# Kernel optimization log

Hardware: AMD Instinct MI355X
Metric: run time of the kernel (lower is better)

The kernel has to match this reference:

```python
import jax, jax.numpy as jnp
import numpy as np

B, T, D, H = 1024, 128, 128, 8
HS = D // H  # 16, matches the hard-coded 16**-0.5 scale
EPS = 1e-5


def setup_inputs() -> dict:
    key = jax.random.key(0)
    ks = jax.random.split(key, 12)
    s = 0.02
    return {
        "x": jax.random.normal(ks[0], (B, T, D), jnp.float32),
        "Wq": jax.random.normal(ks[1], (H, D, HS), jnp.float32) * s,
        "Wk": jax.random.normal(ks[2], (H, D, HS), jnp.float32) * s,
        "Wv": jax.random.normal(ks[3], (H, D, HS), jnp.float32) * s,
        "Wo": jax.random.normal(ks[4], (D, D), jnp.float32) * s,
        "bo": jnp.zeros((D,), jnp.float32),
        "W1": jax.random.normal(ks[5], (D, 4 * D), jnp.float32) * s,
        "b1": jnp.zeros((4 * D,), jnp.float32),
        "W2": jax.random.normal(ks[6], (4 * D, D), jnp.float32) * s,
        "b2": jnp.zeros((D,), jnp.float32),
        "g1": jnp.ones((D,), jnp.float32),
        "be1": jnp.zeros((D,), jnp.float32),
        "g2": jnp.ones((D,), jnp.float32),
        "be2": jnp.zeros((D,), jnp.float32),
    }


def _layernorm(x, g, b):
    mu = jnp.mean(x, axis=-1, keepdims=True)
    var = jnp.mean(jnp.square(x - mu), axis=-1, keepdims=True)
    return (x - mu) * jax.lax.rsqrt(var + EPS) * g + b


def _block(x, Wq, Wk, Wv, Wo, bo, W1, b1, W2, b2, g1, be1, g2, be2):
    h = _layernorm(x, g1, be1)
    q = jnp.einsum('btd,hde->bhte', h, Wq)
    k = jnp.einsum('btd,hde->bhte', h, Wk)
    v = jnp.einsum('btd,hde->bhte', h, Wv)
    scores = jnp.einsum('bhte,bhse->bhts', q, k) * (16.0 ** -0.5)
    causal = jnp.tril(jnp.ones((T, T), bool))
    scores = jnp.where(causal, scores, -jnp.inf)
    wei = jax.nn.softmax(scores, axis=-1)  # dropout off (eval)
    o = jnp.einsum('bhts,bhse->bhte', wei, v)
    o = jnp.transpose(o, (0, 2, 1, 3)).reshape(x.shape[0], T, D)  # concat heads
    x = x + (o @ Wo + bo)
    h2 = _layernorm(x, g2, be2)
    ff = jax.nn.relu(h2 @ W1 + b1) @ W2 + b2
    return x + ff


def reference(x, Wq, Wk, Wv, Wo, bo, W1, b1, W2, b2, g1, be1, g2, be2):
    return _block(x, Wq, Wk, Wv, Wo, bo, W1, b1, W2, b2, g1, be1, g2, be2)
```

## Files before the change

### kernel.cpp

```cpp
#include <hip/hip_runtime.h>
#include <hip/hip_bf16.h>

typedef unsigned short u16;
typedef unsigned int u32;
typedef __bf16 bf16x8 __attribute__((ext_vector_type(8)));
typedef float f32x4 __attribute__((ext_vector_type(4)));

#define LDA 136

__device__ __forceinline__ u16 f2b(float f) {
  __bf16 b = (__bf16)f;
  return __builtin_bit_cast(u16, b);
}
__device__ __forceinline__ float b2f(u16 h) {
  u32 u = ((u32)h) << 16;
  return __builtin_bit_cast(float, u);
}
__device__ __forceinline__ u32 pk2(float lo, float hi) {
  return (u32)f2b(lo) | ((u32)f2b(hi) << 16);
}
__device__ __forceinline__ bf16x8 zero8() {
  union { int4 i; bf16x8 v; } u;
  u.i = make_int4(0, 0, 0, 0);
  return u.v;
}
__device__ __forceinline__ f32x4 mfma16(bf16x8 a, bf16x8 b, f32x4 c) {
  return __builtin_amdgcn_mfma_f32_16x16x32_bf16(a, b, c, 0, 0, 0);
}

__device__ __forceinline__ bf16x8 gatherB(const f32x4& ve, const f32x4& vo,
                                          bool odd_valid, float scale,
                                          int l15, int lg) {
  u32 pe0 = pk2(ve[0] * scale, ve[1] * scale);
  u32 pe1 = pk2(ve[2] * scale, ve[3] * scale);
  u32 po0 = 0, po1 = 0;
  if (odd_valid) {
    po0 = pk2(vo[0] * scale, vo[1] * scale);
    po1 = pk2(vo[2] * scale, vo[3] * scale);
  }
  int s0 = ((lg & 1) * 2) * 16 + l15;
  u32 a0 = __shfl(pe0, s0),      a1 = __shfl(pe1, s0);
  u32 a2 = __shfl(pe0, s0 + 16), a3 = __shfl(pe1, s0 + 16);
  u32 b0 = __shfl(po0, s0),      b1 = __shfl(po1, s0);
  u32 b2 = __shfl(po0, s0 + 16), b3 = __shfl(po1, s0 + 16);
  union { u32 u[4]; bf16x8 v; } fr;
  bool lo = (lg < 2);
  fr.u[0] = lo ? a0 : b0; fr.u[1] = lo ? a1 : b1;
  fr.u[2] = lo ? a2 : b2; fr.u[3] = lo ? a3 : b3;
  return fr.v;
}

__global__ void prep_kernel(const float* __restrict__ Wq, const float* __restrict__ Wk,
                            const float* __restrict__ Wv, const float* __restrict__ Wo,
                            const float* __restrict__ W1, const float* __restrict__ W2,
                            u16* __restrict__ o) {
  int i = blockIdx.x * 256 + threadIdx.x;
  if (i >= 196608) return;
  float v;
  if (i < 49152) {
    int which = i >> 14, j = i & 16383;
    int n = j >> 7, k = j & 127;
    const float* W = (which == 0) ? Wq : (which == 1) ? Wk : Wv;
    v = W[((n >> 4) * 128 + k) * 16 + (n & 15)];
  } else if (i < 65536) {
    int j = i - 49152;
    v = Wo[(j & 127) * 128 + (j >> 7)];
  } else if (i < 131072) {
    int j = i - 65536;
    v = W1[(j & 127) * 512 + (j >> 7)];
  } else {
    int j = i - 131072;
    int c = j & 127, r = (j >> 7) & 15, nt = (j >> 11) & 7, cc = j >> 14;
    v = W2[(cc * 128 + c) * 128 + nt * 16 + r];
  }
  o[i] = f2b(v);
}

__device__ __forceinline__ void ln_regs(const float (&v)[8][4], const float* __restrict__ g,
                                        const float* __restrict__ be,
                                        u16* __restrict__ dst, int r0, int l15) {
  #pragma unroll
  for (int rg = 0; rg < 4; ++rg) {
    float s = 0.f;
    #pragma unroll
    for (int nt = 0; nt < 8; ++nt) s += v[nt][rg];
    s += __shfl_xor(s, 1); s += __shfl_xor(s, 2);
    s += __shfl_xor(s, 4); s += __shfl_xor(s, 8);
    float mu = s * 0.0078125f;
    float vv = 0.f;
    #pragma unroll
    for (int nt = 0; nt < 8; ++nt) { float d = v[nt][rg] - mu; vv += d * d; }
    vv += __shfl_xor(vv, 1); vv += __shfl_xor(vv, 2);
    vv += __shfl_xor(vv, 4); vv += __shfl_xor(vv, 8);
    float rs = rsqrtf(vv * 0.0078125f + 1e-5f);
    #pragma unroll
    for (int nt = 0; nt < 8; ++nt) {
      int col = nt * 16 + l15;
      dst[(r0 + rg) * LDA + col] = f2b((v[nt][rg] - mu) * rs * g[col] + be[col]);
    }
  }
}

__global__ void __launch_bounds__(512, 4)
tblock_kernel(const float* __restrict__ xg, const u16* __restrict__ wts,
              const float* __restrict__ bo, const float* __restrict__ b1,
              const float* __restrict__ b2, const float* __restrict__ g1,
              const float* __restrict__ be1, const float* __restrict__ g2,
              const float* __restrict__ be2, float* __restrict__ out) {
  extern __shared__ u16 sm[];
  u16* buf1 = sm;
  u16* buf2 = sm + 128 * LDA;

  const int tid  = threadIdx.x;
  const int w    = tid >> 6;
  const int lane = tid & 63;
  const int l15  = lane & 15;
  const int lg   = lane >> 4;
  const int r0   = w * 16 + lg * 4;

  const u16* WqT = wts;
  const u16* WkT = wts + 16384;
  const u16* WvT = wts + 32768;
  const u16* WoT = wts + 49152;
  const u16* W1T = wts + 65536;
  const u16* W2S = wts + 131072;

  const float* xp = xg + (size_t)blockIdx.x * 16384;
  float*       op = out + (size_t)blockIdx.x * 16384;

  const f32x4 zf4 = {0.f, 0.f, 0.f, 0.f};
  const bf16x8 zb8 = zero8();

  {
    float xr[8][4];
    #pragma unroll
    for (int nt = 0; nt < 8; ++nt)
      #pragma unroll
      for (int rg = 0; rg < 4; ++rg)
        xr[nt][rg] = xp[(r0 + rg) * 128 + nt * 16 + l15];
    ln_regs(xr, g1, be1, buf1, r0, l15);
  }
  __syncthreads();

  bf16x8 av[4];
  {
    bf16x8 bw[4];
    #pragma unroll
    for (int kk = 0; kk < 4; ++kk)
      bw[kk] = *(const bf16x8*)(WvT + (w * 16 + l15) * 128 + kk * 32 + lg * 8);
    f32x4 va[8];
    #pragma unroll
    for (int mt = 0; mt < 8; ++mt) {
      va[mt] = zf4;
      #pragma unroll
      for (int kk = 0; kk < 4; ++kk)
        va[mt] = mfma16(*(const bf16x8*)(buf1 + (mt * 16 + l15) * LDA + kk * 32 + lg * 8),
                        bw[kk], va[mt]);
    }
    #pragma unroll
    for (int kk = 0; kk < 4; ++kk)
      av[kk] = gatherB(va[2 * kk], va[2 * kk + 1], true, 1.f, l15, lg);
  }

  bf16x8 bk[8];
  {
    bf16x8 bw[4];
    #pragma unroll
    for (int kk = 0; kk < 4; ++kk)
      bw[kk] = *(const bf16x8*)(WkT + (w * 16 + l15) * 128 + kk * 32 + lg * 8);
    f32x4 ka[8];
    #pragma unroll
    for (int mt = 0; mt < 8; ++mt) {
      ka[mt] = zf4;
      #pragma unroll
      for (int kk = 0; kk < 4; ++kk)
        ka[mt] = mfma16(*(const bf16x8*)(buf1 + (mt * 16 + l15) * LDA + kk * 32 + lg * 8),
                        bw[kk], ka[mt]);
    }
    #pragma unroll
    for (int mt = 0; mt < 8; ++mt)
      #pragma unroll
      for (int rg = 0; rg < 4; ++rg)
        buf2[(mt * 16 + lg * 4 + rg) * LDA + w * 16 + l15] = f2b(ka[mt][rg]);
  }
  __syncthreads();
  #pragma unroll
  for (int st = 0; st < 8; ++st) {
    bk[st] = zb8;
    if (lg < 2) bk[st] = *(const bf16x8*)(buf2 + (st * 16 + l15) * LDA + w * 16 + lg * 8);
  }
  __syncthreads();

  {
    bf16x8 bw[4];
    #pragma unroll
    for (int kk = 0; kk < 4; ++kk)
      bw[kk] = *(const bf16x8*)(WqT + (w * 16 + l15) * 128 + kk * 32 + lg * 8);
    f32x4 qa[8];
    #pragma unroll
    for (int mt = 0; mt < 8; ++mt) {
      qa[mt] = zf4;
      #pragma unroll
      for (int kk = 0; kk < 4; ++kk)
        qa[mt] = mfma16(*(const bf16x8*)(buf1 + (mt * 16 + l15) * LDA + kk * 32 + lg * 8),
                        bw[kk], qa[mt]);
    }
    #pragma unroll
    for (int mt = 0; mt < 8; ++mt)
      #pragma unroll
      for (int rg = 0; rg < 4; ++rg)
        buf2[(mt * 16 + lg * 4 + rg) * LDA + w * 16 + l15] = f2b(qa[mt][rg]);
  }
  __syncthreads();

  #pragma unroll 1
  for (int mt = 0; mt < 8; ++mt) {
    bf16x8 aq = zb8;
    if (lg < 2) aq = *(const bf16x8*)(buf2 + (mt * 16 + l15) * LDA + w * 16 + lg * 8);

    f32x4 sacc[8];
    #pragma unroll
    for (int st = 0; st < 8; ++st)
      sacc[st] = (st <= mt) ? mfma16(bk[st], aq, zf4) : zf4;

    float mx = -3.0e38f;
    #pragma unroll
    for (int st = 0; st < 8; ++st) if (st <= mt) {
      #pragma unroll
      for (int rg = 0; rg < 4; ++rg) {
        float sv = sacc[st][rg] * 0.25f;
        bool ok = (st < mt) || ((lg * 4 + rg) <= l15);
        sv = ok ? sv : -1.0e30f;
        sacc[st][rg] = sv;
        mx = fmaxf(mx, sv);
      }
    }
    mx = fmaxf(mx, __shfl_xor(mx, 16));
    mx = fmaxf(mx, __shfl_xor(mx, 32));
    float sum = 0.f;
    #pragma unroll
    for (int st = 0; st < 8; ++st) if (st <= mt) {
      #pragma unroll
      for (int rg = 0; rg < 4; ++rg) {
        float e = __expf(sacc[st][rg] - mx);
        sacc[st][rg] = e;
        sum += e;
      }
    }
    sum += __shfl_xor(sum, 16);
    sum += __shfl_xor(sum, 32);
    float inv = 1.f / sum;

    f32x4 oacc = zf4;
    #pragma unroll
    for (int kk = 0; kk < 4; ++kk) if (kk <= (mt >> 1)) {
      bf16x8 fr = gatherB(sacc[2 * kk], sacc[2 * kk + 1], (2 * kk + 1) <= mt, inv, l15, lg);
      oacc = mfma16(av[kk], fr, oacc);
    }
    union { u16 h[4]; ushort4 s4; } ow;
    #pragma unroll
    for (int rg = 0; rg < 4; ++rg) ow.h[rg] = f2b(oacc[rg]);
    *(ushort4*)(buf2 + (mt * 16 + l15) * LDA + w * 16 + lg * 4) = ow.s4;
  }
  __syncthreads();

  {
    bf16x8 bw[4];
    #pragma unroll
    for (int kk = 0; kk < 4; ++kk)
      bw[kk] = *(const bf16x8*)(WoT + (w * 16 + l15) * 128 + kk * 32 + lg * 8);
    float bov = bo[w * 16 + l15];
    #pragma unroll
    for (int mt = 0; mt < 8; ++mt) {
      float xrl[4];
      #pragma unroll
      for (int rg = 0; rg < 4; ++rg)
        xrl[rg] = xp[(mt * 16 + lg * 4 + rg) * 128 + w * 16 + l15];
      f32x4 acc = zf4;
      #pragma unroll
      for (int kk = 0; kk < 4; ++kk)
        acc = mfma16(*(const bf16x8*)(buf2 + (mt * 16 + l15) * LDA + kk * 32 + lg * 8),
                     bw[kk], acc);
      #pragma unroll
      for (int rg = 0; rg < 4; ++rg) {
        float x1v = acc[rg] + bov + xrl[rg];
        int row = mt * 16 + lg * 4 + rg;
        op[row * 128 + w * 16 + l15] = x1v;
        buf1[row * LDA + w * 16 + l15] = f2b(x1v);
      }
    }
  }
  __syncthreads();

  {
    int rw  = w * 16 + (lane >> 2);
    int sub = lane & 3;
    u16* rp = buf1 + rw * LDA;
    float tv[32];
    float s = 0.f;
    #pragma unroll
    for (int j = 0; j < 32; ++j) { tv[j] = b2f(rp[sub + 4 * j]); s += tv[j]; }
    s += __shfl_xor(s, 1); s += __shfl_xor(s, 2);
    float mu = s * 0.0078125f;
    float vv = 0.f;
    #pragma unroll
    for (int j = 0; j < 32; ++j) { float d = tv[j] - mu; vv += d * d; }
    vv += __shfl_xor(vv, 1); vv += __shfl_xor(vv, 2);
    float rs = rsqrtf(vv * 0.0078125f + 1e-5f);
    #pragma unroll
    for (int j = 0; j < 32; ++j) {
      int c = sub + 4 * j;
      rp[c] = f2b((tv[j] - mu) * rs * g2[c] + be2[c]);
    }
  }
  __syncthreads();

  {
    f32x4 oacc2[8];
    #pragma unroll
    for (int mt = 0; mt < 8; ++mt) oacc2[mt] = zf4;

    #pragma unroll 1
    for (int cc = 0; cc < 4; ++cc) {
      bf16x8 bw1[4];
      #pragma unroll
      for (int kk = 0; kk < 4; ++kk)
        bw1[kk] = *(const bf16x8*)(W1T + (cc * 128 + w * 16 + l15) * 128 + kk * 32 + lg * 8);
      float b1v = b1[cc * 128 + w * 16 + l15];
      #pragma unroll
      for (int mt = 0; mt < 8; ++mt) {
        f32x4 facc = zf4;
        #pragma unroll
        for (int kk = 0; kk < 4; ++kk)
          facc = mfma16(*(const bf16x8*)(buf1 + (mt * 16 + l15) * LDA + kk * 32 + lg * 8),
                        bw1[kk], facc);
        #pragma unroll
        for (int rg = 0; rg < 4; ++rg)
          buf2[(mt * 16 + lg * 4 + rg) * LDA + w * 16 + l15] =
              f2b(fmaxf(facc[rg] + b1v, 0.f));
      }
      __syncthreads();

      bf16x8 bw2[4];
      #pragma unroll
      for (int kk = 0; kk < 4; ++kk)
        bw2[kk] = *(const bf16x8*)(W2S + ((cc * 8 + w) * 16 + l15) * 128 + kk * 32 + lg * 8);
      #pragma unroll
      for (int mt = 0; mt < 8; ++mt)
        #pragma unroll
        for (int kk = 0; kk < 4; ++kk)
          oacc2[mt] = mfma16(*(const bf16x8*)(buf2 + (mt * 16 + l15) * LDA + kk * 32 + lg * 8),
                             bw2[kk], oacc2[mt]);
      __syncthreads();
    }

    float b2v = b2[w * 16 + l15];
    #pragma unroll
    for (int mt = 0; mt < 8; ++mt) {
      float x1r[4];
      #pragma unroll
      for (int rg = 0; rg < 4; ++rg)
        x1r[rg] = op[(mt * 16 + lg * 4 + rg) * 128 + w * 16 + l15];
      #pragma unroll
      for (int rg = 0; rg < 4; ++rg)
        op[(mt * 16 + lg * 4 + rg) * 128 + w * 16 + l15] = oacc2[mt][rg] + b2v + x1r[rg];
    }
  }
}

extern "C" void kernel_launch(void* const* d_in, const int* in_sizes, int n_in,
                              void* d_out, int out_size, void* d_ws, size_t ws_size,
                              hipStream_t stream) {
  const float* x   = (const float*)d_in[0];
  const float* Wq  = (const float*)d_in[1];
  const float* Wk  = (const float*)d_in[2];
  const float* Wv  = (const float*)d_in[3];
  const float* Wo  = (const float*)d_in[4];
  const float* bo  = (const float*)d_in[5];
  const float* W1  = (const float*)d_in[6];
  const float* b1  = (const float*)d_in[7];
  const float* W2  = (const float*)d_in[8];
  const float* b2  = (const float*)d_in[9];
  const float* g1  = (const float*)d_in[10];
  const float* be1 = (const float*)d_in[11];
  const float* g2  = (const float*)d_in[12];
  const float* be2 = (const float*)d_in[13];
  u16* wts = (u16*)d_ws;

  prep_kernel<<<768, 256, 0, stream>>>(Wq, Wk, Wv, Wo, W1, W2, wts);

  const int smem_bytes = 2 * 128 * LDA * 2;
  hipFuncSetAttribute(reinterpret_cast<const void*>(tblock_kernel),
                      hipFuncAttributeMaxDynamicSharedMemorySize, smem_bytes);
  tblock_kernel<<<1024, 512, smem_bytes, stream>>>(x, wts, bo, b1, b2, g1, be1, g2,
                                                   be2, (float*)d_out);
}
```

Baseline: 144.6 us.

## Retile GEMMs as 2x4 warp grid with transposed MFMA and vectorized IO

Each warp now owns a 64-row by 32-column output tile for the Wo, W1 and W2 GEMMs instead of a 16-column strip over all 128 rows. Operand order is swapped so accumulators map to contiguous columns, which allows float4 and ushort4 global and LDS accesses. Q/K/V projections are fused into one pass over the LN output with fewer barriers. The first residual is kept in registers rather than written to and re-read from global, and W2 is re-laid out. Register pressure rises with the larger per-warp tiles, which could lower occupancy.

```diff
diff --git a/kernel.cpp b/kernel.cpp
--- a/kernel.cpp
+++ b/kernel.cpp
@@ -26,6 +26,10 @@
 }
 __device__ __forceinline__ f32x4 mfma16(bf16x8 a, bf16x8 b, f32x4 c) {
   return __builtin_amdgcn_mfma_f32_16x16x32_bf16(a, b, c, 0, 0, 0);
+}
+__device__ __forceinline__ ushort4 pk4(float a, float b, float c, float d) {
+  ushort4 r; r.x = f2b(a); r.y = f2b(b); r.z = f2b(c); r.w = f2b(d);
+  return r;
 }
 
 __device__ __forceinline__ bf16x8 gatherB(const f32x4& ve, const f32x4& vo,
@@ -70,35 +74,10 @@
     v = W1[(j & 127) * 512 + (j >> 7)];
   } else {
     int j = i - 131072;
-    int c = j & 127, r = (j >> 7) & 15, nt = (j >> 11) & 7, cc = j >> 14;
-    v = W2[(cc * 128 + c) * 128 + nt * 16 + r];
+    int c = j >> 9, n = j & 511;
+    v = W2[n * 128 + c];
   }
   o[i] = f2b(v);
-}
-
-__device__ __forceinline__ void ln_regs(const float (&v)[8][4], const float* __restrict__ g,
-                                        const float* __restrict__ be,
-                                        u16* __restrict__ dst, int r0, int l15) {
-  #pragma unroll
-  for (int rg = 0; rg < 4; ++rg) {
-    float s = 0.f;
-    #pragma unroll
-    for (int nt = 0; nt < 8; ++nt) s += v[nt][rg];
-    s += __shfl_xor(s, 1); s += __shfl_xor(s, 2);
-    s += __shfl_xor(s, 4); s += __shfl_xor(s, 8);
-    float mu = s * 0.0078125f;
-    float vv = 0.f;
-    #pragma unroll
-    for (int nt = 0; nt < 8; ++nt) { float d = v[nt][rg] - mu; vv += d * d; }
-    vv += __shfl_xor(vv, 1); vv += __shfl_xor(vv, 2);
-    vv += __shfl_xor(vv, 4); vv += __shfl_xor(vv, 8);
-    float rs = rsqrtf(vv * 0.0078125f + 1e-5f);
-    #pragma unroll
-    for (int nt = 0; nt < 8; ++nt) {
-      int col = nt * 16 + l15;
-      dst[(r0 + rg) * LDA + col] = f2b((v[nt][rg] - mu) * rs * g[col] + be[col]);
-    }
-  }
 }
 
 __global__ void __launch_bounds__(512, 4)
@@ -116,14 +95,17 @@
   const int lane = tid & 63;
   const int l15  = lane & 15;
   const int lg   = lane >> 4;
-  const int r0   = w * 16 + lg * 4;
-
-  const u16* WqT = wts;
-  const u16* WkT = wts + 16384;
-  const u16* WvT = wts + 32768;
-  const u16* WoT = wts + 49152;
-  const u16* W1T = wts + 65536;
-  const u16* W2S = wts + 131072;
+  const int mr   = w >> 2;
+  const int nc   = w & 3;
+  const int tr0  = mr * 64;
+  const int cb   = nc * 32;
+
+  const u16* WqT  = wts;
+  const u16* WkT  = wts + 16384;
+  const u16* WvT  = wts + 32768;
+  const u16* WoT  = wts + 49152;
+  const u16* W1T  = wts + 65536;
+  const u16* W2T2 = wts + 131072;
 
   const float* xp = xg + (size_t)blockIdx.x * 16384;
   float*       op = out + (size_t)blockIdx.x * 16384;
@@ -132,91 +114,89 @@
   const bf16x8 zb8 = zero8();
 
   {
-    float xr[8][4];
+    const int t = w * 16 + l15;
+    float v[8][4];
+    #pragma unroll
+    for (int nt = 0; nt < 8; ++nt) {
+      float4 f = *(const float4*)(xp + t * 128 + nt * 16 + lg * 4);
+      v[nt][0] = f.x; v[nt][1] = f.y; v[nt][2] = f.z; v[nt][3] = f.w;
+    }
+    float s = 0.f;
     #pragma unroll
     for (int nt = 0; nt < 8; ++nt)
       #pragma unroll
-      for (int rg = 0; rg < 4; ++rg)
-        xr[nt][rg] = xp[(r0 + rg) * 128 + nt * 16 + l15];
-    ln_regs(xr, g1, be1, buf1, r0, l15);
+      for (int r = 0; r < 4; ++r) s += v[nt][r];
+    s += __shfl_xor(s, 16); s += __shfl_xor(s, 32);
+    float mu = s * 0.0078125f;
+    float vv = 0.f;
+    #pragma unroll
+    for (int nt = 0; nt < 8; ++nt)
+      #pragma unroll
+      for (int r = 0; r < 4; ++r) { float d = v[nt][r] - mu; vv += d * d; }
+    vv += __shfl_xor(vv, 16); vv += __shfl_xor(vv, 32);
+    float rs = rsqrtf(vv * 0.0078125f + 1e-5f);
+    #pragma unroll
+    for (int nt = 0; nt < 8; ++nt) {
+      float4 gv = *(const float4*)(g1 + nt * 16 + lg * 4);
+      float4 bv = *(const float4*)(be1 + nt * 16 + lg * 4);
+      *(ushort4*)(buf1 + t * LDA + nt * 16 + lg * 4) =
+          pk4((v[nt][0] - mu) * rs * gv.x + bv.x, (v[nt][1] - mu) * rs * gv.y + bv.y,
+              (v[nt][2] - mu) * rs * gv.z + bv.z, (v[nt][3] - mu) * rs * gv.w + bv.w);
+    }
   }
   __syncthreads();
 
   bf16x8 av[4];
-  {
-    bf16x8 bw[4];
-    #pragma unroll
-    for (int kk = 0; kk < 4; ++kk)
-      bw[kk] = *(const bf16x8*)(WvT + (w * 16 + l15) * 128 + kk * 32 + lg * 8);
-    f32x4 va[8];
-    #pragma unroll
-    for (int mt = 0; mt < 8; ++mt) {
-      va[mt] = zf4;
-      #pragma unroll
-      for (int kk = 0; kk < 4; ++kk)
-        va[mt] = mfma16(*(const bf16x8*)(buf1 + (mt * 16 + l15) * LDA + kk * 32 + lg * 8),
-                        bw[kk], va[mt]);
-    }
-    #pragma unroll
-    for (int kk = 0; kk < 4; ++kk)
-      av[kk] = gatherB(va[2 * kk], va[2 * kk + 1], true, 1.f, l15, lg);
-  }
-
   bf16x8 bk[8];
   {
-    bf16x8 bw[4];
-    #pragma unroll
-    for (int kk = 0; kk < 4; ++kk)
-      bw[kk] = *(const bf16x8*)(WkT + (w * 16 + l15) * 128 + kk * 32 + lg * 8);
-    f32x4 ka[8];
+    bf16x8 wq[4], wk[4], wv[4];
+    #pragma unroll
+    for (int kk = 0; kk < 4; ++kk) {
+      wq[kk] = *(const bf16x8*)(WqT + (w * 16 + l15) * 128 + kk * 32 + lg * 8);
+      wk[kk] = *(const bf16x8*)(WkT + (w * 16 + l15) * 128 + kk * 32 + lg * 8);
+      wv[kk] = *(const bf16x8*)(WvT + (w * 16 + l15) * 128 + kk * 32 + lg * 8);
+    }
+    u32 qp[8][2];
+    f32x4 vprev = zf4;
     #pragma unroll
     for (int mt = 0; mt < 8; ++mt) {
-      ka[mt] = zf4;
+      bf16x8 hf[4];
       #pragma unroll
       for (int kk = 0; kk < 4; ++kk)
-        ka[mt] = mfma16(*(const bf16x8*)(buf1 + (mt * 16 + l15) * LDA + kk * 32 + lg * 8),
-                        bw[kk], ka[mt]);
-    }
-    #pragma unroll
-    for (int mt = 0; mt < 8; ++mt)
-      #pragma unroll
-      for (int rg = 0; rg < 4; ++rg)
-        buf2[(mt * 16 + lg * 4 + rg) * LDA + w * 16 + l15] = f2b(ka[mt][rg]);
-  }
-  __syncthreads();
-  #pragma unroll
-  for (int st = 0; st < 8; ++st) {
-    bk[st] = zb8;
-    if (lg < 2) bk[st] = *(const bf16x8*)(buf2 + (st * 16 + l15) * LDA + w * 16 + lg * 8);
-  }
-  __syncthreads();
-
-  {
-    bf16x8 bw[4];
-    #pragma unroll
-    for (int kk = 0; kk < 4; ++kk)
-      bw[kk] = *(const bf16x8*)(WqT + (w * 16 + l15) * 128 + kk * 32 + lg * 8);
-    f32x4 qa[8];
+        hf[kk] = *(const bf16x8*)(buf1 + (mt * 16 + l15) * LDA + kk * 32 + lg * 8);
+      f32x4 va = zf4, ka = zf4, qa = zf4;
+      #pragma unroll
+      for (int kk = 0; kk < 4; ++kk) {
+        va = mfma16(hf[kk], wv[kk], va);
+        ka = mfma16(wk[kk], hf[kk], ka);
+        qa = mfma16(wq[kk], hf[kk], qa);
+      }
+      *(ushort4*)(buf2 + (mt * 16 + l15) * LDA + w * 16 + lg * 4) =
+          pk4(ka[0], ka[1], ka[2], ka[3]);
+      qp[mt][0] = pk2(qa[0], qa[1]);
+      qp[mt][1] = pk2(qa[2], qa[3]);
+      if (mt & 1) av[mt >> 1] = gatherB(vprev, va, true, 1.f, l15, lg);
+      else        vprev = va;
+    }
+    #pragma unroll
+    for (int st = 0; st < 8; ++st) {
+      bk[st] = zb8;
+      if (lg < 2)
+        bk[st] = *(const bf16x8*)(buf2 + (st * 16 + l15) * LDA + w * 16 + lg * 8);
+    }
     #pragma unroll
     for (int mt = 0; mt < 8; ++mt) {
-      qa[mt] = zf4;
-      #pragma unroll
-      for (int kk = 0; kk < 4; ++kk)
-        qa[mt] = mfma16(*(const bf16x8*)(buf1 + (mt * 16 + l15) * LDA + kk * 32 + lg * 8),
-                        bw[kk], qa[mt]);
-    }
-    #pragma unroll
-    for (int mt = 0; mt < 8; ++mt)
-      #pragma unroll
-      for (int rg = 0; rg < 4; ++rg)
-        buf2[(mt * 16 + lg * 4 + rg) * LDA + w * 16 + l15] = f2b(qa[mt][rg]);
-  }
-  __syncthreads();
+      union { u32 u[2]; ushort4 s; } uq;
+      uq.u[0] = qp[mt][0]; uq.u[1] = qp[mt][1];
+      *(ushort4*)(buf2 + (mt * 16 + l15) * LDA + w * 16 + lg * 4) = uq.s;
+    }
+  }
 
   #pragma unroll 1
   for (int mt = 0; mt < 8; ++mt) {
     bf16x8 aq = zb8;
-    if (lg < 2) aq = *(const bf16x8*)(buf2 + (mt * 16 + l15) * LDA + w * 16 + lg * 8);
+    if (lg < 2)
+      aq = *(const bf16x8*)(buf2 + (mt * 16 + l15) * LDA + w * 16 + lg * 8);
 
     f32x4 sacc[8];
     #pragma unroll
@@ -257,113 +237,148 @@
       bf16x8 fr = gatherB(sacc[2 * kk], sacc[2 * kk + 1], (2 * kk + 1) <= mt, inv, l15, lg);
       oacc = mfma16(av[kk], fr, oacc);
     }
-    union { u16 h[4]; ushort4 s4; } ow;
-    #pragma unroll
-    for (int rg = 0; rg < 4; ++rg) ow.h[rg] = f2b(oacc[rg]);
-    *(ushort4*)(buf2 + (mt * 16 + l15) * LDA + w * 16 + lg * 4) = ow.s4;
+    *(ushort4*)(buf2 + (mt * 16 + l15) * LDA + w * 16 + lg * 4) =
+        pk4(oacc[0], oacc[1], oacc[2], oacc[3]);
   }
   __syncthreads();
 
+  f32x4 x1r[4][2];
   {
-    bf16x8 bw[4];
-    #pragma unroll
-    for (int kk = 0; kk < 4; ++kk)
-      bw[kk] = *(const bf16x8*)(WoT + (w * 16 + l15) * 128 + kk * 32 + lg * 8);
-    float bov = bo[w * 16 + l15];
-    #pragma unroll
-    for (int mt = 0; mt < 8; ++mt) {
-      float xrl[4];
-      #pragma unroll
-      for (int rg = 0; rg < 4; ++rg)
-        xrl[rg] = xp[(mt * 16 + lg * 4 + rg) * 128 + w * 16 + l15];
-      f32x4 acc = zf4;
+    bf16x8 wo[2][4];
+    #pragma unroll
+    for (int ct = 0; ct < 2; ++ct)
       #pragma unroll
       for (int kk = 0; kk < 4; ++kk)
-        acc = mfma16(*(const bf16x8*)(buf2 + (mt * 16 + l15) * LDA + kk * 32 + lg * 8),
-                     bw[kk], acc);
-      #pragma unroll
-      for (int rg = 0; rg < 4; ++rg) {
-        float x1v = acc[rg] + bov + xrl[rg];
-        int row = mt * 16 + lg * 4 + rg;
-        op[row * 128 + w * 16 + l15] = x1v;
-        buf1[row * LDA + w * 16 + l15] = f2b(x1v);
+        wo[ct][kk] = *(const bf16x8*)(WoT + (cb + ct * 16 + l15) * 128 + kk * 32 + lg * 8);
+    #pragma unroll
+    for (int mt = 0; mt < 4; ++mt) {
+      const int t = tr0 + mt * 16 + l15;
+      bf16x8 ofr[4];
+      #pragma unroll
+      for (int kk = 0; kk < 4; ++kk)
+        ofr[kk] = *(const bf16x8*)(buf2 + t * LDA + kk * 32 + lg * 8);
+      #pragma unroll
+      for (int ct = 0; ct < 2; ++ct) {
+        f32x4 acc = zf4;
+        #pragma unroll
+        for (int kk = 0; kk < 4; ++kk)
+          acc = mfma16(wo[ct][kk], ofr[kk], acc);
+        float4 xv = *(const float4*)(xp + t * 128 + cb + ct * 16 + lg * 4);
+        float4 bv = *(const float4*)(bo + cb + ct * 16 + lg * 4);
+        x1r[mt][ct][0] = acc[0] + bv.x + xv.x;
+        x1r[mt][ct][1] = acc[1] + bv.y + xv.y;
+        x1r[mt][ct][2] = acc[2] + bv.z + xv.z;
+        x1r[mt][ct][3] = acc[3] + bv.w + xv.w;
+        *(ushort4*)(buf1 + t * LDA + cb + ct * 16 + lg * 4) =
+            pk4(x1r[mt][ct][0], x1r[mt][ct][1], x1r[mt][ct][2], x1r[mt][ct][3]);
       }
     }
   }
   __syncthreads();
 
   {
-    int rw  = w * 16 + (lane >> 2);
-    int sub = lane & 3;
-    u16* rp = buf1 + rw * LDA;
-    float tv[32];
+    const int t = w * 16 + l15;
+    float v[8][4];
+    #pragma unroll
+    for (int nt = 0; nt < 8; ++nt) {
+      ushort4 u = *(const ushort4*)(buf1 + t * LDA + nt * 16 + lg * 4);
+      v[nt][0] = b2f(u.x); v[nt][1] = b2f(u.y); v[nt][2] = b2f(u.z); v[nt][3] = b2f(u.w);
+    }
     float s = 0.f;
     #pragma unroll
-    for (int j = 0; j < 32; ++j) { tv[j] = b2f(rp[sub + 4 * j]); s += tv[j]; }
-    s += __shfl_xor(s, 1); s += __shfl_xor(s, 2);
+    for (int nt = 0; nt < 8; ++nt)
+      #pragma unroll
+      for (int r = 0; r < 4; ++r) s += v[nt][r];
+    s += __shfl_xor(s, 16); s += __shfl_xor(s, 32);
     float mu = s * 0.0078125f;
     float vv = 0.f;
     #pragma unroll
-    for (int j = 0; j < 32; ++j) { float d = tv[j] - mu; vv += d * d; }
-    vv += __shfl_xor(vv, 1); vv += __shfl_xor(vv, 2);
+    for (int nt = 0; nt < 8; ++nt)
+      #pragma unroll
+      for (int r = 0; r < 4; ++r) { float d = v[nt][r] - mu; vv += d * d; }
+    vv += __shfl_xor(vv, 16); vv += __shfl_xor(vv, 32);
     float rs = rsqrtf(vv * 0.0078125f + 1e-5f);
     #pragma unroll
-    for (int j = 0; j < 32; ++j) {
-      int c = sub + 4 * j;
-      rp[c] = f2b((tv[j] - mu) * rs * g2[c] + be2[c]);
+    for (int nt = 0; nt < 8; ++nt) {
+      float4 gv = *(const float4*)(g2 + nt * 16 + lg * 4);
+      float4 bv = *(const float4*)(be2 + nt * 16 + lg * 4);
+      *(ushort4*)(buf1 + t * LDA + nt * 16 + lg * 4) =
+          pk4((v[nt][0] - mu) * rs * gv.x + bv.x, (v[nt][1] - mu) * rs * gv.y + bv.y,
+              (v[nt][2] - mu) * rs * gv.z + bv.z, (v[nt][3] - mu) * rs * gv.w + bv.w);
     }
   }
   __syncthreads();
 
   {
-    f32x4 oacc2[8];
-    #pragma unroll
-    for (int mt = 0; mt < 8; ++mt) oacc2[mt] = zf4;
+    f32x4 oacc[4][2];
+    #pragma unroll
+    for (int mt = 0; mt < 4; ++mt)
+      #pragma unroll
+      for (int ct = 0; ct < 2; ++ct) oacc[mt][ct] = zf4;
 
     #pragma unroll 1
     for (int cc = 0; cc < 4; ++cc) {
-      bf16x8 bw1[4];
-      #pragma unroll
-      for (int kk = 0; kk < 4; ++kk)
-        bw1[kk] = *(const bf16x8*)(W1T + (cc * 128 + w * 16 + l15) * 128 + kk * 32 + lg * 8);
-      float b1v = b1[cc * 128 + w * 16 + l15];
-      #pragma unroll
-      for (int mt = 0; mt < 8; ++mt) {
-        f32x4 facc = zf4;
+      bf16x8 w1f[2][4];
+      #pragma unroll
+      for (int ct = 0; ct < 2; ++ct)
         #pragma unroll
         for (int kk = 0; kk < 4; ++kk)
-          facc = mfma16(*(const bf16x8*)(buf1 + (mt * 16 + l15) * LDA + kk * 32 + lg * 8),
-                        bw1[kk], facc);
-        #pragma unroll
-        for (int rg = 0; rg < 4; ++rg)
-          buf2[(mt * 16 + lg * 4 + rg) * LDA + w * 16 + l15] =
-              f2b(fmaxf(facc[rg] + b1v, 0.f));
+          w1f[ct][kk] = *(const bf16x8*)(W1T + (cc * 128 + cb + ct * 16 + l15) * 128 + kk * 32 + lg * 8);
+      #pragma unroll
+      for (int mt = 0; mt < 4; ++mt) {
+        const int t = tr0 + mt * 16 + l15;
+        bf16x8 h2f[4];
+        #pragma unroll
+        for (int kk = 0; kk < 4; ++kk)
+          h2f[kk] = *(const bf16x8*)(buf1 + t * LDA + kk * 32 + lg * 8);
+        #pragma unroll
+        for (int ct = 0; ct < 2; ++ct) {
+          f32x4 fa = zf4;
+          #pragma unroll
+          for (int kk = 0; kk < 4; ++kk)
+            fa = mfma16(w1f[ct][kk], h2f[kk], fa);
+          float4 bv = *(const float4*)(b1 + cc * 128 + cb + ct * 16 + lg * 4);
+          *(ushort4*)(buf2 + t * LDA + cb + ct * 16 + lg * 4) =
+              pk4(fmaxf(fa[0] + bv.x, 0.f), fmaxf(fa[1] + bv.y, 0.f),
+                  fmaxf(fa[2] + bv.z, 0.f), fmaxf(fa[3] + bv.w, 0.f));
+        }
       }
       __syncthreads();
 
-      bf16x8 bw2[4];
-      #pragma unroll
-      for (int kk = 0; kk < 4; ++kk)
-        bw2[kk] = *(const bf16x8*)(W2S + ((cc * 8 + w) * 16 + l15) * 128 + kk * 32 + lg * 8);
-      #pragma unroll
-      for (int mt = 0; mt < 8; ++mt)
+      bf16x8 w2f[2][4];
+      #pragma unroll
+      for (int ct = 0; ct < 2; ++ct)
         #pragma unroll
         for (int kk = 0; kk < 4; ++kk)
-          oacc2[mt] = mfma16(*(const bf16x8*)(buf2 + (mt * 16 + l15) * LDA + kk * 32 + lg * 8),
-                             bw2[kk], oacc2[mt]);
-      __syncthreads();
-    }
-
-    float b2v = b2[w * 16 + l15];
-    #pragma unroll
-    for (int mt = 0; mt < 8; ++mt) {
-      float x1r[4];
-      #pragma unroll
-      for (int rg = 0; rg < 4; ++rg)
-        x1r[rg] = op[(mt * 16 + lg * 4 + rg) * 128 + w * 16 + l15];
-      #pragma unroll
-      for (int rg = 0; rg < 4; ++rg)
-        op[(mt * 16 + lg * 4 + rg) * 128 + w * 16 + l15] = oacc2[mt][rg] + b2v + x1r[rg];
+          w2f[ct][kk] = *(const bf16x8*)(W2T2 + (cb + ct * 16 + l15) * 512 + cc * 128 + kk * 32 + lg * 8);
+      #pragma unroll
+      for (int mt = 0; mt < 4; ++mt) {
+        bf16x8 rf[4];
+        #pragma unroll
+        for (int kk = 0; kk < 4; ++kk)
+          rf[kk] = *(const bf16x8*)(buf2 + (tr0 + mt * 16 + l15) * LDA + kk * 32 + lg * 8);
+        #pragma unroll
+        for (int ct = 0; ct < 2; ++ct)
+          #pragma unroll
+          for (int kk = 0; kk < 4; ++kk)
+            oacc[mt][ct] = mfma16(w2f[ct][kk], rf[kk], oacc[mt][ct]);
+      }
+      if (cc < 3) __syncthreads();
+    }
+
+    #pragma unroll
+    for (int mt = 0; mt < 4; ++mt) {
+      const int t = tr0 + mt * 16 + l15;
+      #pragma unroll
+      for (int ct = 0; ct < 2; ++ct) {
+        float4 bv = *(const float4*)(b2 + cb + ct * 16 + lg * 4);
+        float4 st;
+        st.x = oacc[mt][ct][0] + bv.x + x1r[mt][ct][0];
+        st.y = oacc[mt][ct][1] + bv.y + x1r[mt][ct][1];
+        st.z = oacc[mt][ct][2] + bv.z + x1r[mt][ct][2];
+        st.w = oacc[mt][ct][3] + bv.w + x1r[mt][ct][3];
+        *(float4*)(op + t * 128 + cb + ct * 16 + lg * 4) = st;
+      }
     }
   }
 }
```

Result: slower. 165.6 us (+14.5%).

## Drop per-warp-local barriers, keep residual in registers, vectorize layernorms

Applied to the files above, without the earlier changes.

Removes barriers around the K/Q staging in the shared buffer, since each warp only reads the columns it wrote itself. The post-attention residual plus b2 now stays in the FFN accumulator registers instead of being written to global memory and read back at the end. Both layernorms switch to a one-row-per-16-lanes layout with float4/ushort4 vector loads and stores. The V and K/Q projections now accumulate one tile at a time, and the final FFN barrier is skipped. The trade-off is higher register pressure, because the accumulators stay live through LN2 under a tight launch-bounds budget, which risks spills.

```diff
diff --git a/kernel.cpp b/kernel.cpp
--- a/kernel.cpp
+++ b/kernel.cpp
@@ -26,6 +26,10 @@
 }
 __device__ __forceinline__ f32x4 mfma16(bf16x8 a, bf16x8 b, f32x4 c) {
   return __builtin_amdgcn_mfma_f32_16x16x32_bf16(a, b, c, 0, 0, 0);
+}
+__device__ __forceinline__ ushort4 pk4(float a, float b, float c, float d) {
+  ushort4 r; r.x = f2b(a); r.y = f2b(b); r.z = f2b(c); r.w = f2b(d);
+  return r;
 }
 
 __device__ __forceinline__ bf16x8 gatherB(const f32x4& ve, const f32x4& vo,
@@ -76,31 +80,6 @@
   o[i] = f2b(v);
 }
 
-__device__ __forceinline__ void ln_regs(const float (&v)[8][4], const float* __restrict__ g,
-                                        const float* __restrict__ be,
-                                        u16* __restrict__ dst, int r0, int l15) {
-  #pragma unroll
-  for (int rg = 0; rg < 4; ++rg) {
-    float s = 0.f;
-    #pragma unroll
-    for (int nt = 0; nt < 8; ++nt) s += v[nt][rg];
-    s += __shfl_xor(s, 1); s += __shfl_xor(s, 2);
-    s += __shfl_xor(s, 4); s += __shfl_xor(s, 8);
-    float mu = s * 0.0078125f;
-    float vv = 0.f;
-    #pragma unroll
-    for (int nt = 0; nt < 8; ++nt) { float d = v[nt][rg] - mu; vv += d * d; }
-    vv += __shfl_xor(vv, 1); vv += __shfl_xor(vv, 2);
-    vv += __shfl_xor(vv, 4); vv += __shfl_xor(vv, 8);
-    float rs = rsqrtf(vv * 0.0078125f + 1e-5f);
-    #pragma unroll
-    for (int nt = 0; nt < 8; ++nt) {
-      int col = nt * 16 + l15;
-      dst[(r0 + rg) * LDA + col] = f2b((v[nt][rg] - mu) * rs * g[col] + be[col]);
-    }
-  }
-}
-
 __global__ void __launch_bounds__(512, 4)
 tblock_kernel(const float* __restrict__ xg, const u16* __restrict__ wts,
               const float* __restrict__ bo, const float* __restrict__ b1,
@@ -116,7 +95,6 @@
   const int lane = tid & 63;
   const int l15  = lane & 15;
   const int lg   = lane >> 4;
-  const int r0   = w * 16 + lg * 4;
 
   const u16* WqT = wts;
   const u16* WkT = wts + 16384;
@@ -132,13 +110,35 @@
   const bf16x8 zb8 = zero8();
 
   {
-    float xr[8][4];
+    const int t = w * 16 + l15;
+    float v[8][4];
+    #pragma unroll
+    for (int nt = 0; nt < 8; ++nt) {
+      float4 f = *(const float4*)(xp + t * 128 + nt * 16 + lg * 4);
+      v[nt][0] = f.x; v[nt][1] = f.y; v[nt][2] = f.z; v[nt][3] = f.w;
+    }
+    float s = 0.f;
     #pragma unroll
     for (int nt = 0; nt < 8; ++nt)
       #pragma unroll
-      for (int rg = 0; rg < 4; ++rg)
-        xr[nt][rg] = xp[(r0 + rg) * 128 + nt * 16 + l15];
-    ln_regs(xr, g1, be1, buf1, r0, l15);
+      for (int r = 0; r < 4; ++r) s += v[nt][r];
+    s += __shfl_xor(s, 16); s += __shfl_xor(s, 32);
+    float mu = s * 0.0078125f;
+    float vv = 0.f;
+    #pragma unroll
+    for (int nt = 0; nt < 8; ++nt)
+      #pragma unroll
+      for (int r = 0; r < 4; ++r) { float d = v[nt][r] - mu; vv += d * d; }
+    vv += __shfl_xor(vv, 16); vv += __shfl_xor(vv, 32);
+    float rs = rsqrtf(vv * 0.0078125f + 1e-5f);
+    #pragma unroll
+    for (int nt = 0; nt < 8; ++nt) {
+      float4 gv = *(const float4*)(g1 + nt * 16 + lg * 4);
+      float4 bv = *(const float4*)(be1 + nt * 16 + lg * 4);
+      *(ushort4*)(buf1 + t * LDA + nt * 16 + lg * 4) =
+          pk4((v[nt][0] - mu) * rs * gv.x + bv.x, (v[nt][1] - mu) * rs * gv.y + bv.y,
+              (v[nt][2] - mu) * rs * gv.z + bv.z, (v[nt][3] - mu) * rs * gv.w + bv.w);
+    }
   }
   __syncthreads();
 
@@ -148,75 +148,67 @@
     #pragma unroll
     for (int kk = 0; kk < 4; ++kk)
       bw[kk] = *(const bf16x8*)(WvT + (w * 16 + l15) * 128 + kk * 32 + lg * 8);
-    f32x4 va[8];
+    f32x4 vprev = zf4;
     #pragma unroll
     for (int mt = 0; mt < 8; ++mt) {
-      va[mt] = zf4;
-      #pragma unroll
-      for (int kk = 0; kk < 4; ++kk)
-        va[mt] = mfma16(*(const bf16x8*)(buf1 + (mt * 16 + l15) * LDA + kk * 32 + lg * 8),
-                        bw[kk], va[mt]);
-    }
-    #pragma unroll
-    for (int kk = 0; kk < 4; ++kk)
-      av[kk] = gatherB(va[2 * kk], va[2 * kk + 1], true, 1.f, l15, lg);
-  }
-
-  bf16x8 bk[8];
+      f32x4 va = zf4;
+      #pragma unroll
+      for (int kk = 0; kk < 4; ++kk)
+        va = mfma16(*(const bf16x8*)(buf1 + (mt * 16 + l15) * LDA + kk * 32 + lg * 8),
+                    bw[kk], va);
+      if (mt & 1) av[mt >> 1] = gatherB(vprev, va, true, 1.f, l15, lg);
+      else        vprev = va;
+    }
+  }
+
   {
     bf16x8 bw[4];
     #pragma unroll
     for (int kk = 0; kk < 4; ++kk)
       bw[kk] = *(const bf16x8*)(WkT + (w * 16 + l15) * 128 + kk * 32 + lg * 8);
-    f32x4 ka[8];
     #pragma unroll
     for (int mt = 0; mt < 8; ++mt) {
-      ka[mt] = zf4;
-      #pragma unroll
-      for (int kk = 0; kk < 4; ++kk)
-        ka[mt] = mfma16(*(const bf16x8*)(buf1 + (mt * 16 + l15) * LDA + kk * 32 + lg * 8),
-                        bw[kk], ka[mt]);
-    }
-    #pragma unroll
-    for (int mt = 0; mt < 8; ++mt)
+      f32x4 ka = zf4;
+      #pragma unroll
+      for (int kk = 0; kk < 4; ++kk)
+        ka = mfma16(*(const bf16x8*)(buf1 + (mt * 16 + l15) * LDA + kk * 32 + lg * 8),
+                    bw[kk], ka);
       #pragma unroll
       for (int rg = 0; rg < 4; ++rg)
-        buf2[(mt * 16 + lg * 4 + rg) * LDA + w * 16 + l15] = f2b(ka[mt][rg]);
-  }
-  __syncthreads();
+        buf2[(mt * 16 + lg * 4 + rg) * LDA + w * 16 + l15] = f2b(ka[rg]);
+    }
+  }
+  bf16x8 bk[8];
   #pragma unroll
   for (int st = 0; st < 8; ++st) {
     bk[st] = zb8;
-    if (lg < 2) bk[st] = *(const bf16x8*)(buf2 + (st * 16 + l15) * LDA + w * 16 + lg * 8);
-  }
-  __syncthreads();
+    if (lg < 2)
+      bk[st] = *(const bf16x8*)(buf2 + (st * 16 + l15) * LDA + w * 16 + lg * 8);
+  }
 
   {
     bf16x8 bw[4];
     #pragma unroll
     for (int kk = 0; kk < 4; ++kk)
       bw[kk] = *(const bf16x8*)(WqT + (w * 16 + l15) * 128 + kk * 32 + lg * 8);
-    f32x4 qa[8];
     #pragma unroll
     for (int mt = 0; mt < 8; ++mt) {
-      qa[mt] = zf4;
-      #pragma unroll
-      for (int kk = 0; kk < 4; ++kk)
-        qa[mt] = mfma16(*(const bf16x8*)(buf1 + (mt * 16 + l15) * LDA + kk * 32 + lg * 8),
-                        bw[kk], qa[mt]);
-    }
-    #pragma unroll
-    for (int mt = 0; mt < 8; ++mt)
+      f32x4 qa = zf4;
+      #pragma unroll
+      for (int kk = 0; kk < 4; ++kk)
+        qa = mfma16(*(const bf16x8*)(buf1 + (mt * 16 + l15) * LDA + kk * 32 + lg * 8),
+                    bw[kk], qa);
       #pragma unroll
       for (int rg = 0; rg < 4; ++rg)
-        buf2[(mt * 16 + lg * 4 + rg) * LDA + w * 16 + l15] = f2b(qa[mt][rg]);
-  }
-  __syncthreads();
+        buf2[(mt * 16 + lg * 4 + rg) * LDA + w * 16 + l15] = f2b(qa[rg]);
+    }
+  }
 
   #pragma unroll 1
   for (int mt = 0; mt < 8; ++mt) {
     bf16x8 aq = zb8;
-    if (lg < 2) aq = *(const bf16x8*)(buf2 + (mt * 16 + l15) * LDA + w * 16 + lg * 8);
+    if (lg < 2)
+      aq = *(const bf16x8*)(buf2 + (mt * 16 + l15) * LDA + w * 16 + lg * 8);
 
     f32x4 sacc[8];
     #pragma unroll
@@ -251,25 +243,25 @@
     sum += __shfl_xor(sum, 32);
     float inv = 1.f / sum;
 
-    f32x4 oacc = zf4;
+    f32x4 oa = zf4;
     #pragma unroll
     for (int kk = 0; kk < 4; ++kk) if (kk <= (mt >> 1)) {
       bf16x8 fr = gatherB(sacc[2 * kk], sacc[2 * kk + 1], (2 * kk + 1) <= mt, inv, l15, lg);
-      oacc = mfma16(av[kk], fr, oacc);
-    }
-    union { u16 h[4]; ushort4 s4; } ow;
-    #pragma unroll
-    for (int rg = 0; rg < 4; ++rg) ow.h[rg] = f2b(oacc[rg]);
-    *(ushort4*)(buf2 + (mt * 16 + l15) * LDA + w * 16 + lg * 4) = ow.s4;
+      oa = mfma16(av[kk], fr, oa);
+    }
+    *(ushort4*)(buf2 + (mt * 16 + l15) * LDA + w * 16 + lg * 4) =
+        pk4(oa[0], oa[1], oa[2], oa[3]);
   }
   __syncthreads();
 
+  f32x4 oacc2[8];
   {
     bf16x8 bw[4];
     #pragma unroll
     for (int kk = 0; kk < 4; ++kk)
       bw[kk] = *(const bf16x8*)(WoT + (w * 16 + l15) * 128 + kk * 32 + lg * 8);
     float bov = bo[w * 16 + l15];
+    float b2v = b2[w * 16 + l15];
     #pragma unroll
     for (int mt = 0; mt < 8; ++mt) {
       float xrl[4];
@@ -284,44 +276,49 @@
       #pragma unroll
       for (int rg = 0; rg < 4; ++rg) {
         float x1v = acc[rg] + bov + xrl[rg];
-        int row = mt * 16 + lg * 4 + rg;
-        op[row * 128 + w * 16 + l15] = x1v;
-        buf1[row * LDA + w * 16 + l15] = f2b(x1v);
+        buf1[(mt * 16 + lg * 4 + rg) * LDA + w * 16 + l15] = f2b(x1v);
+        oacc2[mt][rg] = x1v + b2v;
       }
     }
   }
   __syncthreads();
 
   {
-    int rw  = w * 16 + (lane >> 2);
-    int sub = lane & 3;
-    u16* rp = buf1 + rw * LDA;
-    float tv[32];
+    const int t = w * 16 + l15;
+    float v[8][4];
+    #pragma unroll
+    for (int nt = 0; nt < 8; ++nt) {
+      ushort4 u = *(const ushort4*)(buf1 + t * LDA + nt * 16 + lg * 4);
+      v[nt][0] = b2f(u.x); v[nt][1] = b2f(u.y); v[nt][2] = b2f(u.z); v[nt][3] = b2f(u.w);
+    }
     float s = 0.f;
     #pragma unroll
-    for (int j = 0; j < 32; ++j) { tv[j] = b2f(rp[sub + 4 * j]); s += tv[j]; }
-    s += __shfl_xor(s, 1); s += __shfl_xor(s, 2);
+    for (int nt = 0; nt < 8; ++nt)
+      #pragma unroll
+      for (int r = 0; r < 4; ++r) s += v[nt][r];
+    s += __shfl_xor(s, 16); s += __shfl_xor(s, 32);
     float mu = s * 0.0078125f;
     float vv = 0.f;
     #pragma unroll
-    for (int j = 0; j < 32; ++j) { float d = tv[j] - mu; vv += d * d; }
-    vv += __shfl_xor(vv, 1); vv += __shfl_xor(vv, 2);
+    for (int nt = 0; nt < 8; ++nt)
+      #pragma unroll
+      for (int r = 0; r < 4; ++r) { float d = v[nt][r] - mu; vv += d * d; }
+    vv += __shfl_xor(vv, 16); vv += __shfl_xor(vv, 32);
     float rs = rsqrtf(vv * 0.0078125f + 1e-5f);
     #pragma unroll
-    for (int j = 0; j < 32; ++j) {
-      int c = sub + 4 * j;
-      rp[c] = f2b((tv[j] - mu) * rs * g2[c] + be2[c]);
+    for (int nt = 0; nt < 8; ++nt) {
+      float4 gv = *(const float4*)(g2 + nt * 16 + lg * 4);
+      float4 bv = *(const float4*)(be2 + nt * 16 + lg * 4);
+      *(ushort4*)(buf1 + t * LDA + nt * 16 + lg * 4) =
+          pk4((v[nt][0] - mu) * rs * gv.x + bv.x, (v[nt][1] - mu) * rs * gv.y + bv.y,
+              (v[nt][2] - mu) * rs * gv.z + bv.z, (v[nt][3] - mu) * rs * gv.w + bv.w);
     }
   }
   __syncthreads();
 
-  {
-    f32x4 oacc2[8];
-    #pragma unroll
-    for (int mt = 0; mt < 8; ++mt) oacc2[mt] = zf4;
-
-    #pragma unroll 1
-    for (int cc = 0; cc < 4; ++cc) {
+  #pragma unroll 1
+  for (int cc = 0; cc < 4; ++cc) {
+    {
       bf16x8 bw1[4];
       #pragma unroll
       for (int kk = 0; kk < 4; ++kk)
@@ -339,8 +336,10 @@
           buf2[(mt * 16 + lg * 4 + rg) * LDA + w * 16 + l15] =
               f2b(fmaxf(facc[rg] + b1v, 0.f));
       }
-      __syncthreads();
-
+    }
+    __syncthreads();
+
+    {
       bf16x8 bw2[4];
       #pragma unroll
       for (int kk = 0; kk < 4; ++kk)
@@ -351,21 +350,15 @@
         for (int kk = 0; kk < 4; ++kk)
           oacc2[mt] = mfma16(*(const bf16x8*)(buf2 + (mt * 16 + l15) * LDA + kk * 32 + lg * 8),
                              bw2[kk], oacc2[mt]);
-      __syncthreads();
-    }
-
-    float b2v = b2[w * 16 + l15];
-    #pragma unroll
-    for (int mt = 0; mt < 8; ++mt) {
-      float x1r[4];
-      #pragma unroll
-      for (int rg = 0; rg < 4; ++rg)
-        x1r[rg] = op[(mt * 16 + lg * 4 + rg) * 128 + w * 16 + l15];
-      #pragma unroll
-      for (int rg = 0; rg < 4; ++rg)
-        op[(mt * 16 + lg * 4 + rg) * 128 + w * 16 + l15] = oacc2[mt][rg] + b2v + x1r[rg];
-    }
-  }
+    }
+    if (cc < 3) __syncthreads();
+  }
+
+  #pragma unroll
+  for (int mt = 0; mt < 8; ++mt)
+    #pragma unroll
+    for (int rg = 0; rg < 4; ++rg)
+      op[(mt * 16 + lg * 4 + rg) * 128 + w * 16 + l15] = oacc2[mt][rg];
 }
 
 extern "C" void kernel_launch(void* const* d_in, const int* in_sizes, int n_in,
```

After: 145.0 us. Within noise of the previous version (+0.2%).
